# Optimization experiments

Hardware: AMD Instinct MI355X
Metric: run time of the kernel (lower is better)

Reference implementation:

```python
import jax, jax.numpy as jnp
import numpy as np

N = 50000      # nodes
E = 800000     # edges (before self loops)
NG = 512       # graphs in batch
D_IN = 128
D_H = 128
D_FC = 128
D_OUT = 2


def _gcn_conv(x, src, dst, norm, W, b, num_nodes):
    # x: [N, d_in] -> [N, d_out]; symmetric-normalized scatter-add over edges
    h = x @ W                              # [N, d_out]
    msg = h[src] * norm[:, None]           # [E+N, d_out]
    out = jax.ops.segment_sum(msg, dst, num_segments=num_nodes)
    return out + b


def setup_inputs() -> dict:
    key = jax.random.key(0)
    ks = jax.random.split(key, 12)
    x = jax.random.normal(ks[0], (N, D_IN), dtype=jnp.float32)
    edge_index = jax.random.randint(ks[1], (2, E), 0, N, dtype=jnp.int64)
    batch = jnp.sort(jax.random.randint(ks[2], (N,), 0, NG, dtype=jnp.int64))

    def glorot(k, shape):
        lim = float(np.sqrt(6.0 / (shape[0] + shape[1])))
        return jax.random.uniform(k, shape, jnp.float32, -lim, lim)

    return {
        "x": x, "edge_index": edge_index, "batch": batch,
        "W1": glorot(ks[3], (D_IN, D_H)), "b1": jnp.zeros((D_H,), jnp.float32),
        "W2": glorot(ks[4], (D_H, D_H)), "b2": jnp.zeros((D_H,), jnp.float32),
        "Wf1": glorot(ks[5], (D_H, D_FC)), "bf1": jnp.zeros((D_FC,), jnp.float32),
        "Wf2": glorot(ks[6], (D_FC, D_OUT)), "bf2": jnp.zeros((D_OUT,), jnp.float32),
    }


def reference(x, edge_index, batch, W1, b1, W2, b2, Wf1, bf1, Wf2, bf2):
    # add self loops (PyG GCNConv default)
    loops = jnp.arange(N, dtype=edge_index.dtype)
    src = jnp.concatenate([edge_index[0], loops])   # [E+N]
    dst = jnp.concatenate([edge_index[1], loops])   # [E+N]
    deg = jax.ops.segment_sum(jnp.ones_like(dst, dtype=x.dtype), dst, num_segments=N)
    dinv = jax.lax.rsqrt(deg)                       # deg >= 1 due to self loops
    norm = dinv[src] * dinv[dst]                    # [E+N]

    h = jax.nn.relu(_gcn_conv(x, src, dst, norm, W1, b1, N))
    h = jax.nn.relu(_gcn_conv(h, src, dst, norm, W2, b2, N))

    # global mean pool over graphs
    sums = jax.ops.segment_sum(h, batch, num_segments=NG)          # [NG, D_H]
    cnts = jax.ops.segment_sum(jnp.ones((N,), h.dtype), batch, num_segments=NG)
    g = sums / jnp.maximum(cnts, 1.0)[:, None]

    z = jax.nn.relu(g @ Wf1 + bf1)
    return z @ Wf2 + bf2
```

## Files before the change

### kernel.cpp

```cpp
#include <hip/hip_runtime.h>

typedef __attribute__((ext_vector_type(8))) short short8;
typedef __attribute__((ext_vector_type(4))) float f32x4;

__device__ __forceinline__ unsigned short f2b(float x) {
  unsigned u = __float_as_uint(x);
  u += 0x7FFF + ((u >> 16) & 1);
  return (unsigned short)(u >> 16);
}
__device__ __forceinline__ float b2f_lo(unsigned v) { return __uint_as_float(v << 16); }
__device__ __forceinline__ float b2f_hi(unsigned v) { return __uint_as_float(v & 0xFFFF0000u); }

#define EPB 4096
#define BKT 256
#define RPW 32

__global__ __launch_bounds__(256) void k_setup(
    const float* __restrict__ W1, unsigned short* __restrict__ Wt1,
    const float* __restrict__ W2, unsigned short* __restrict__ Wt2,
    const int* __restrict__ dst, int E, int nbuck, int* __restrict__ mat)
{
  __shared__ float tile[32][33];
  __shared__ int h[256];
  int t = threadIdx.x;
  if (blockIdx.x < 32) {
    const float* W = (blockIdx.x < 16) ? W1 : W2;
    unsigned short* Wt = (blockIdx.x < 16) ? Wt1 : Wt2;
    int bid = blockIdx.x & 15;
    int tx = t & 31, ty = t >> 5;
    int bx = bid & 3, by = bid >> 2;
    #pragma unroll
    for (int i = 0; i < 4; ++i)
      tile[ty + i * 8][tx] = W[(by * 32 + ty + i * 8) * 128 + bx * 32 + tx];
    __syncthreads();
    #pragma unroll
    for (int i = 0; i < 4; ++i)
      Wt[(bx * 32 + ty + i * 8) * 128 + by * 32 + tx] = f2b(tile[tx][ty + i * 8]);
  } else {
    int blk = blockIdx.x - 32;
    h[t] = 0;
    __syncthreads();
    int e0 = blk * EPB, e1 = min(e0 + EPB, E);
    for (int e = e0 + t; e < e1; e += 256) atomicAdd(&h[dst[e] >> 8], 1);
    __syncthreads();
    if (t < nbuck) mat[blk * nbuck + t] = h[t];
  }
}

__global__ __launch_bounds__(256) void k_excl(const int* __restrict__ mat, int neb, int nbuck,
                                              int* __restrict__ boff, int* __restrict__ cursor,
                                              int* __restrict__ rowptr, int N_) {
  __shared__ int s[256];
  int t = threadIdx.x;
  int sum = 0;
  if (t < nbuck) {
    #pragma unroll 8
    for (int r = 0; r < neb; ++r) sum += mat[r * nbuck + t];
  }
  s[t] = sum;
  __syncthreads();
  #pragma unroll
  for (int d = 1; d < 256; d <<= 1) {
    int u = (t >= d) ? s[t - d] : 0;
    __syncthreads();
    s[t] += u;
    __syncthreads();
  }
  if (t < nbuck) { boff[t] = s[t] - sum; cursor[t] = s[t] - sum; }
  if (t == 0) { boff[nbuck] = s[255]; rowptr[N_] = s[255]; }
}

__global__ __launch_bounds__(256) void k_part(const int* __restrict__ src,
                                              const int* __restrict__ dst, int E, int nbuck,
                                              const int* __restrict__ mat,
                                              int* __restrict__ cursor,
                                              unsigned* __restrict__ staged,
                                              float* __restrict__ sums,
                                              int* __restrict__ cnt, int ng) {
  __shared__ int cur[256];
  int t = threadIdx.x;
  if (t < nbuck) {
    int c = mat[blockIdx.x * nbuck + t];
    cur[t] = c ? atomicAdd(&cursor[t], c) : 0;
  }
  __syncthreads();
  int e0 = blockIdx.x * EPB, e1 = min(e0 + EPB, E);
  for (int e = e0 + t; e < e1; e += 256) {
    int d = dst[e];
    int pos = atomicAdd(&cur[d >> 8], 1);
    staged[pos] = ((unsigned)(d & 255) << 16) | (unsigned)src[e];
  }
  int tot_e = ng * 128;
  for (int i = blockIdx.x * 256 + t; i < tot_e; i += gridDim.x * 256) sums[i] = 0.f;
  for (int i = blockIdx.x * 256 + t; i < ng; i += gridDim.x * 256) cnt[i] = 0;
}

__global__ __launch_bounds__(256) void k_csr(const unsigned* __restrict__ staged,
                                             const int* __restrict__ boff, int N_,
                                             float* __restrict__ dinv, int* __restrict__ rowptr,
                                             unsigned short* __restrict__ csr16) {
  __shared__ int cnt[256];
  __shared__ int cur[256];
  int b = blockIdx.x, t = threadIdx.x;
  int lo = boff[b], hi = boff[b + 1];
  cnt[t] = 0;
  __syncthreads();
  for (int i = lo + t; i < hi; i += 256) atomicAdd(&cnt[staged[i] >> 16], 1);
  __syncthreads();
  int v = cnt[t];
  #pragma unroll
  for (int d = 1; d < 256; d <<= 1) {
    int u = (t >= d) ? cnt[t - d] : 0;
    __syncthreads();
    cnt[t] += u;
    __syncthreads();
  }
  int start = lo + cnt[t] - v;
  cur[t] = start;
  int node = (b << 8) + t;
  if (node < N_) {
    rowptr[node] = start;
    dinv[node] = rsqrtf((float)(v + 1));
  }
  __syncthreads();
  for (int i = lo + t; i < hi; i += 256) {
    unsigned e = staged[i];
    int pos = atomicAdd(&cur[e >> 16], 1);
    csr16[pos] = (unsigned short)(e & 0xFFFFu);
  }
}

template<int A_F32>
__global__ __launch_bounds__(256) void k_mfma_gemm(
    const void* __restrict__ Ap, const unsigned short* __restrict__ Wt,
    const float* __restrict__ dinv, unsigned short* __restrict__ Out, int M)
{
  int wv = threadIdx.x >> 6, lane = threadIdx.x & 63;
  int kb = (lane >> 4) * 8;
  short8 bf[8][4];
  const unsigned short* Bc = Wt + (size_t)(lane & 15) * 128 + kb;
  #pragma unroll
  for (int ct = 0; ct < 8; ++ct)
    #pragma unroll
    for (int ks = 0; ks < 4; ++ks)
      bf[ct][ks] = *(const short8*)(Bc + ct * 16 * 128 + ks * 32);

  int r0 = (blockIdx.x * 4 + wv) * 32;
  #pragma unroll
  for (int rt = 0; rt < 2; ++rt) {
    int rbase = r0 + rt * 16;
    if (rbase >= M) return;
    int arow = rbase + (lane & 15);
    short8 a[4];
    if (A_F32) {
      const float* Ar = (const float*)Ap + (size_t)arow * 128 + kb;
      #pragma unroll
      for (int ks = 0; ks < 4; ++ks) {
        float4 u = *(const float4*)(Ar + ks * 32);
        float4 v = *(const float4*)(Ar + ks * 32 + 4);
        short8 tt;
        tt[0] = (short)f2b(u.x); tt[1] = (short)f2b(u.y);
        tt[2] = (short)f2b(u.z); tt[3] = (short)f2b(u.w);
        tt[4] = (short)f2b(v.x); tt[5] = (short)f2b(v.y);
        tt[6] = (short)f2b(v.z); tt[7] = (short)f2b(v.w);
        a[ks] = tt;
      }
    } else {
      const unsigned short* Ar = (const unsigned short*)Ap + (size_t)arow * 128 + kb;
      #pragma unroll
      for (int ks = 0; ks < 4; ++ks)
        a[ks] = *(const short8*)(Ar + ks * 32);
    }
    f32x4 acc[8];
    #pragma unroll
    for (int i = 0; i < 8; ++i) acc[i] = (f32x4){0.f, 0.f, 0.f, 0.f};
    #pragma unroll
    for (int ct = 0; ct < 8; ++ct)
      #pragma unroll
      for (int ks = 0; ks < 4; ++ks)
        acc[ct] = __builtin_amdgcn_mfma_f32_16x16x32_bf16(a[ks], bf[ct][ks], acc[ct], 0, 0, 0);
    int orow = rbase + (lane >> 4) * 4;
    int ocol = lane & 15;
    float s0 = dinv[orow], s1 = dinv[orow + 1], s2 = dinv[orow + 2], s3 = dinv[orow + 3];
    #pragma unroll
    for (int ct = 0; ct < 8; ++ct) {
      unsigned short* o = Out + (size_t)orow * 128 + ct * 16 + ocol;
      o[0]   = f2b(acc[ct][0] * s0);
      o[128] = f2b(acc[ct][1] * s1);
      o[256] = f2b(acc[ct][2] * s2);
      o[384] = f2b(acc[ct][3] * s3);
    }
  }
}

__global__ __launch_bounds__(256) void k_gather_post(
    const unsigned short* __restrict__ csr16, const int* __restrict__ rowptr,
    const unsigned short* __restrict__ P, const float* __restrict__ dinv,
    const float* __restrict__ bias, unsigned short* __restrict__ R, int n)
{
  int node = blockIdx.x * 8 + (threadIdx.x >> 5);
  if (node >= n) return;
  int lane = threadIdx.x & 31;
  int lo = rowptr[node], hi = rowptr[node + 1];
  float a0 = 0.f, a1 = 0.f, a2 = 0.f, a3 = 0.f;
  int e = lo;
  for (; e + 8 <= hi; e += 8) {
    int s0 = csr16[e],     s1 = csr16[e + 1], s2 = csr16[e + 2], s3 = csr16[e + 3];
    int s4 = csr16[e + 4], s5 = csr16[e + 5], s6 = csr16[e + 6], s7 = csr16[e + 7];
    uint2 v0 = ((const uint2*)(P + (size_t)s0 * 128))[lane];
    uint2 v1 = ((const uint2*)(P + (size_t)s1 * 128))[lane];
    uint2 v2 = ((const uint2*)(P + (size_t)s2 * 128))[lane];
    uint2 v3 = ((const uint2*)(P + (size_t)s3 * 128))[lane];
    uint2 v4 = ((const uint2*)(P + (size_t)s4 * 128))[lane];
    uint2 v5 = ((const uint2*)(P + (size_t)s5 * 128))[lane];
    uint2 v6 = ((const uint2*)(P + (size_t)s6 * 128))[lane];
    uint2 v7 = ((const uint2*)(P + (size_t)s7 * 128))[lane];
    a0 += b2f_lo(v0.x) + b2f_lo(v1.x) + b2f_lo(v2.x) + b2f_lo(v3.x)
        + b2f_lo(v4.x) + b2f_lo(v5.x) + b2f_lo(v6.x) + b2f_lo(v7.x);
    a1 += b2f_hi(v0.x) + b2f_hi(v1.x) + b2f_hi(v2.x) + b2f_hi(v3.x)
        + b2f_hi(v4.x) + b2f_hi(v5.x) + b2f_hi(v6.x) + b2f_hi(v7.x);
    a2 += b2f_lo(v0.y) + b2f_lo(v1.y) + b2f_lo(v2.y) + b2f_lo(v3.y)
        + b2f_lo(v4.y) + b2f_lo(v5.y) + b2f_lo(v6.y) + b2f_lo(v7.y);
    a3 += b2f_hi(v0.y) + b2f_hi(v1.y) + b2f_hi(v2.y) + b2f_hi(v3.y)
        + b2f_hi(v4.y) + b2f_hi(v5.y) + b2f_hi(v6.y) + b2f_hi(v7.y);
  }
  for (; e + 4 <= hi; e += 4) {
    int s0 = csr16[e], s1 = csr16[e + 1], s2 = csr16[e + 2], s3 = csr16[e + 3];
    uint2 v0 = ((const uint2*)(P + (size_t)s0 * 128))[lane];
    uint2 v1 = ((const uint2*)(P + (size_t)s1 * 128))[lane];
    uint2 v2 = ((const uint2*)(P + (size_t)s2 * 128))[lane];
    uint2 v3 = ((const uint2*)(P + (size_t)s3 * 128))[lane];
    a0 += b2f_lo(v0.x) + b2f_lo(v1.x) + b2f_lo(v2.x) + b2f_lo(v3.x);
    a1 += b2f_hi(v0.x) + b2f_hi(v1.x) + b2f_hi(v2.x) + b2f_hi(v3.x);
    a2 += b2f_lo(v0.y) + b2f_lo(v1.y) + b2f_lo(v2.y) + b2f_lo(v3.y);
    a3 += b2f_hi(v0.y) + b2f_hi(v1.y) + b2f_hi(v2.y) + b2f_hi(v3.y);
  }
  for (; e < hi; ++e) {
    int s = csr16[e];
    uint2 v = ((const uint2*)(P + (size_t)s * 128))[lane];
    a0 += b2f_lo(v.x); a1 += b2f_hi(v.x);
    a2 += b2f_lo(v.y); a3 += b2f_hi(v.y);
  }
  float dv = dinv[node];
  uint2 hv = ((const uint2*)(P + (size_t)node * 128))[lane];
  float4 bb = ((const float4*)bias)[lane];
  float r0 = fmaxf(dv * (a0 + b2f_lo(hv.x)) + bb.x, 0.f);
  float r1 = fmaxf(dv * (a1 + b2f_hi(hv.x)) + bb.y, 0.f);
  float r2 = fmaxf(dv * (a2 + b2f_lo(hv.y)) + bb.z, 0.f);
  float r3 = fmaxf(dv * (a3 + b2f_hi(hv.y)) + bb.w, 0.f);
  uint2 pack;
  pack.x = (unsigned)f2b(r0) | ((unsigned)f2b(r1) << 16);
  pack.y = (unsigned)f2b(r2) | ((unsigned)f2b(r3) << 16);
  ((uint2*)(R + (size_t)node * 128))[lane] = pack;
}

__global__ __launch_bounds__(256) void k_pool_sum(
    const unsigned short* __restrict__ h2, const int* __restrict__ batch, int n,
    float* __restrict__ sums, int* __restrict__ cnt)
{
  int wid = blockIdx.x * 4 + (threadIdx.x >> 6);
  int lane = threadIdx.x & 63;
  int r0 = wid * RPW;
  if (r0 >= n) return;
  int r1 = min(r0 + RPW, n);
  const unsigned* H = (const unsigned*)h2;
  int gcur = batch[r0];
  float ax = 0.f, ay = 0.f;
  int run = 0;
  for (int r = r0; r < r1; ++r) {
    int g = batch[r];
    if (g != gcur) {
      atomicAdd(&sums[(size_t)gcur * 128 + 2 * lane], ax);
      atomicAdd(&sums[(size_t)gcur * 128 + 2 * lane + 1], ay);
      if (lane == 0) atomicAdd(&cnt[gcur], run);
      ax = ay = 0.f; run = 0; gcur = g;
    }
    unsigned v = H[(size_t)r * 64 + lane];
    ax += b2f_lo(v); ay += b2f_hi(v); ++run;
  }
  atomicAdd(&sums[(size_t)gcur * 128 + 2 * lane], ax);
  atomicAdd(&sums[(size_t)gcur * 128 + 2 * lane + 1], ay);
  if (lane == 0) atomicAdd(&cnt[gcur], run);
}

__global__ __launch_bounds__(128) void k_fc(
    const float* __restrict__ sums, const int* __restrict__ cnt,
    const float* __restrict__ Wf1, const float* __restrict__ bf1,
    const float* __restrict__ Wf2, const float* __restrict__ bf2,
    float* __restrict__ out)
{
  __shared__ float gl[128];
  __shared__ float red0[128];
  __shared__ float red1[128];
  int g = blockIdx.x, t = threadIdx.x;
  float c = (float)cnt[g];
  gl[t] = sums[(size_t)g * 128 + t] / fmaxf(c, 1.f);
  __syncthreads();
  float z0 = 0.f, z1 = 0.f, z2 = 0.f, z3 = 0.f;
  #pragma unroll
  for (int k = 0; k < 32; ++k) {
    z0 += gl[k]      * Wf1[k * 128 + t];
    z1 += gl[k + 32] * Wf1[(k + 32) * 128 + t];
    z2 += gl[k + 64] * Wf1[(k + 64) * 128 + t];
    z3 += gl[k + 96] * Wf1[(k + 96) * 128 + t];
  }
  float z = fmaxf((z0 + z1) + (z2 + z3) + bf1[t], 0.f);
  red0[t] = z * Wf2[2 * t];
  red1[t] = z * Wf2[2 * t + 1];
  __syncthreads();
  #pragma unroll
  for (int d = 64; d > 0; d >>= 1) {
    if (t < d) { red0[t] += red0[t + d]; red1[t] += red1[t + d]; }
    __syncthreads();
  }
  if (t == 0) {
    out[g * 2]     = red0[0] + bf2[0];
    out[g * 2 + 1] = red1[0] + bf2[1];
  }
}

extern "C" void kernel_launch(void* const* d_in, const int* in_sizes, int n_in,
                              void* d_out, int out_size, void* d_ws, size_t ws_size,
                              hipStream_t stream) {
  const float* x    = (const float*)d_in[0];
  const int*   ei   = (const int*)d_in[1];
  const int*   batch= (const int*)d_in[2];
  const float* W1   = (const float*)d_in[3];
  const float* b1   = (const float*)d_in[4];
  const float* W2   = (const float*)d_in[5];
  const float* b2   = (const float*)d_in[6];
  const float* Wf1  = (const float*)d_in[7];
  const float* bf1  = (const float*)d_in[8];
  const float* Wf2  = (const float*)d_in[9];
  const float* bf2  = (const float*)d_in[10];
  float* out = (float*)d_out;

  const int N  = in_sizes[0] / 128;
  const int E  = in_sizes[1] / 2;
  const int NG = out_size / 2;
  const int* srcp = ei;
  const int* dstp = ei + E;

  const int nbuck = (N + BKT - 1) / BKT;
  const int neb   = (E + EPB - 1) / EPB;

  char* ws = (char*)d_ws;
  size_t off = 0;
  auto carve = [&](size_t bytes) { void* p = ws + off; off += (bytes + 255) & ~(size_t)255; return p; };
  float* dinv   = (float*)carve((size_t)N * 4);
  int*   rowptr = (int*)  carve((size_t)(N + 1) * 4);
  int*   boff   = (int*)  carve((size_t)(nbuck + 1) * 4);
  int*   cursor = (int*)  carve((size_t)256 * 4);
  int*   mat    = (int*)  carve((size_t)neb * nbuck * 4);
  unsigned*       staged = (unsigned*)      carve((size_t)E * 4);
  unsigned short* csr16  = (unsigned short*)carve((size_t)E * 2);
  unsigned short* Wt1 = (unsigned short*)carve(128 * 128 * 2);
  unsigned short* Wt2 = (unsigned short*)carve(128 * 128 * 2);
  float* sums   = (float*)carve((size_t)NG * 128 * 4);
  int*   cntg   = (int*)  carve((size_t)NG * 4);
  const size_t nb_row = (size_t)N * 128 * 2;
  unsigned short* U0 = (unsigned short*)carve(nb_row);
  unsigned short* U1 = (unsigned short*)carve(nb_row);

  k_setup<<<32 + neb, 256, 0, stream>>>(W1, Wt1, W2, Wt2, dstp, E, nbuck, mat);
  k_excl<<<1, 256, 0, stream>>>(mat, neb, nbuck, boff, cursor, rowptr, N);
  k_part<<<neb, 256, 0, stream>>>(srcp, dstp, E, nbuck, mat, cursor, staged, sums, cntg, NG);
  k_csr <<<nbuck, 256, 0, stream>>>(staged, boff, N, dinv, rowptr, csr16);

  const int gblocks = (N + 127) / 128;
  k_mfma_gemm<1><<<gblocks, 256, 0, stream>>>(x, Wt1, dinv, U0, N);
  k_gather_post<<<(N + 7) / 8, 256, 0, stream>>>(csr16, rowptr, U0, dinv, b1, U1, N);
  k_mfma_gemm<0><<<gblocks, 256, 0, stream>>>(U1, Wt2, dinv, U0, N);
  k_gather_post<<<(N + 7) / 8, 256, 0, stream>>>(csr16, rowptr, U0, dinv, b2, U1, N);

  const int pblocks = (N + RPW * 4 - 1) / (RPW * 4);
  k_pool_sum<<<pblocks, 256, 0, stream>>>(U1, batch, N, sums, cntg);
  k_fc<<<NG, 128, 0, stream>>>(sums, cntg, Wf1, bf1, Wf2, bf2, out);
}
```

Baseline: 160.9 us.

## Fuse CSR build stages into one cooperative kernel with grid syncs

Replaces the four graph-preprocessing launches (bucket histogram/weight transpose, scan, partition, per-bucket CSR) with a single cooperative kernel of 256 blocks that loops over the former block indices and separates stages with grid.sync(). The goal is to remove three kernel launch gaps and their inter-kernel drain. In exchange, each stage now runs on a fixed 256-block grid, so the stages that had more blocks get less parallelism, and the scan stage runs on one block while the rest wait at a grid barrier.

After: 256.9 us. +59.7%, slower.

```diff
diff --git a/kernel.cpp b/kernel.cpp
--- a/kernel.cpp
+++ b/kernel.cpp
@@ -1,4 +1,7 @@
 #include <hip/hip_runtime.h>
+#include <hip/hip_cooperative_groups.h>
+
+namespace cg = cooperative_groups;
 
 typedef __attribute__((ext_vector_type(8))) short short8;
 typedef __attribute__((ext_vector_type(4))) float f32x4;
@@ -15,118 +18,119 @@
 #define BKT 256
 #define RPW 32
 
-__global__ __launch_bounds__(256) void k_setup(
+__global__ __launch_bounds__(256) void k_build(
     const float* __restrict__ W1, unsigned short* __restrict__ Wt1,
     const float* __restrict__ W2, unsigned short* __restrict__ Wt2,
-    const int* __restrict__ dst, int E, int nbuck, int* __restrict__ mat)
-{
+    const int* __restrict__ src, const int* __restrict__ dst,
+    int E, int N_, int nbuck, int neb,
+    int* __restrict__ mat, int* __restrict__ boff, int* __restrict__ cursor,
+    int* __restrict__ rowptr, unsigned* __restrict__ staged,
+    unsigned short* __restrict__ csr16, float* __restrict__ dinv,
+    float* __restrict__ sums, int* __restrict__ cntg, int ng)
+{
+  cg::grid_group grid = cg::this_grid();
   __shared__ float tile[32][33];
-  __shared__ int h[256];
-  int t = threadIdx.x;
-  if (blockIdx.x < 32) {
-    const float* W = (blockIdx.x < 16) ? W1 : W2;
-    unsigned short* Wt = (blockIdx.x < 16) ? Wt1 : Wt2;
-    int bid = blockIdx.x & 15;
-    int tx = t & 31, ty = t >> 5;
-    int bx = bid & 3, by = bid >> 2;
-    #pragma unroll
-    for (int i = 0; i < 4; ++i)
-      tile[ty + i * 8][tx] = W[(by * 32 + ty + i * 8) * 128 + bx * 32 + tx];
-    __syncthreads();
-    #pragma unroll
-    for (int i = 0; i < 4; ++i)
-      Wt[(bx * 32 + ty + i * 8) * 128 + by * 32 + tx] = f2b(tile[tx][ty + i * 8]);
-  } else {
-    int blk = blockIdx.x - 32;
-    h[t] = 0;
-    __syncthreads();
-    int e0 = blk * EPB, e1 = min(e0 + EPB, E);
-    for (int e = e0 + t; e < e1; e += 256) atomicAdd(&h[dst[e] >> 8], 1);
-    __syncthreads();
-    if (t < nbuck) mat[blk * nbuck + t] = h[t];
-  }
-}
-
-__global__ __launch_bounds__(256) void k_excl(const int* __restrict__ mat, int neb, int nbuck,
-                                              int* __restrict__ boff, int* __restrict__ cursor,
-                                              int* __restrict__ rowptr, int N_) {
-  __shared__ int s[256];
-  int t = threadIdx.x;
-  int sum = 0;
-  if (t < nbuck) {
-    #pragma unroll 8
-    for (int r = 0; r < neb; ++r) sum += mat[r * nbuck + t];
-  }
-  s[t] = sum;
-  __syncthreads();
-  #pragma unroll
-  for (int d = 1; d < 256; d <<= 1) {
-    int u = (t >= d) ? s[t - d] : 0;
-    __syncthreads();
-    s[t] += u;
-    __syncthreads();
-  }
-  if (t < nbuck) { boff[t] = s[t] - sum; cursor[t] = s[t] - sum; }
-  if (t == 0) { boff[nbuck] = s[255]; rowptr[N_] = s[255]; }
-}
-
-__global__ __launch_bounds__(256) void k_part(const int* __restrict__ src,
-                                              const int* __restrict__ dst, int E, int nbuck,
-                                              const int* __restrict__ mat,
-                                              int* __restrict__ cursor,
-                                              unsigned* __restrict__ staged,
-                                              float* __restrict__ sums,
-                                              int* __restrict__ cnt, int ng) {
-  __shared__ int cur[256];
-  int t = threadIdx.x;
-  if (t < nbuck) {
-    int c = mat[blockIdx.x * nbuck + t];
-    cur[t] = c ? atomicAdd(&cursor[t], c) : 0;
-  }
-  __syncthreads();
-  int e0 = blockIdx.x * EPB, e1 = min(e0 + EPB, E);
-  for (int e = e0 + t; e < e1; e += 256) {
-    int d = dst[e];
-    int pos = atomicAdd(&cur[d >> 8], 1);
-    staged[pos] = ((unsigned)(d & 255) << 16) | (unsigned)src[e];
-  }
-  int tot_e = ng * 128;
-  for (int i = blockIdx.x * 256 + t; i < tot_e; i += gridDim.x * 256) sums[i] = 0.f;
-  for (int i = blockIdx.x * 256 + t; i < ng; i += gridDim.x * 256) cnt[i] = 0;
-}
-
-__global__ __launch_bounds__(256) void k_csr(const unsigned* __restrict__ staged,
-                                             const int* __restrict__ boff, int N_,
-                                             float* __restrict__ dinv, int* __restrict__ rowptr,
-                                             unsigned short* __restrict__ csr16) {
-  __shared__ int cnt[256];
-  __shared__ int cur[256];
-  int b = blockIdx.x, t = threadIdx.x;
-  int lo = boff[b], hi = boff[b + 1];
-  cnt[t] = 0;
-  __syncthreads();
-  for (int i = lo + t; i < hi; i += 256) atomicAdd(&cnt[staged[i] >> 16], 1);
-  __syncthreads();
-  int v = cnt[t];
-  #pragma unroll
-  for (int d = 1; d < 256; d <<= 1) {
-    int u = (t >= d) ? cnt[t - d] : 0;
-    __syncthreads();
-    cnt[t] += u;
-    __syncthreads();
-  }
-  int start = lo + cnt[t] - v;
-  cur[t] = start;
-  int node = (b << 8) + t;
-  if (node < N_) {
-    rowptr[node] = start;
-    dinv[node] = rsqrtf((float)(v + 1));
-  }
-  __syncthreads();
-  for (int i = lo + t; i < hi; i += 256) {
-    unsigned e = staged[i];
-    int pos = atomicAdd(&cur[e >> 16], 1);
-    csr16[pos] = (unsigned short)(e & 0xFFFFu);
+  __shared__ int ibuf[256];
+  __shared__ int ibuf2[256];
+  const int t = threadIdx.x;
+
+  for (int b = blockIdx.x; b < 32 + neb; b += gridDim.x) {
+    if (b < 32) {
+      const float* W = (b < 16) ? W1 : W2;
+      unsigned short* Wt = (b < 16) ? Wt1 : Wt2;
+      int bid = b & 15;
+      int tx = t & 31, ty = t >> 5;
+      int bx = bid & 3, by = bid >> 2;
+      #pragma unroll
+      for (int i = 0; i < 4; ++i)
+        tile[ty + i * 8][tx] = W[(by * 32 + ty + i * 8) * 128 + bx * 32 + tx];
+      __syncthreads();
+      #pragma unroll
+      for (int i = 0; i < 4; ++i)
+        Wt[(bx * 32 + ty + i * 8) * 128 + by * 32 + tx] = f2b(tile[tx][ty + i * 8]);
+      __syncthreads();
+    } else {
+      int blk = b - 32;
+      ibuf[t] = 0;
+      __syncthreads();
+      int e0 = blk * EPB, e1 = min(e0 + EPB, E);
+      for (int e = e0 + t; e < e1; e += 256) atomicAdd(&ibuf[dst[e] >> 8], 1);
+      __syncthreads();
+      if (t < nbuck) mat[blk * nbuck + t] = ibuf[t];
+      __syncthreads();
+    }
+  }
+  grid.sync();
+
+  if (blockIdx.x == 0) {
+    int sum = 0;
+    if (t < nbuck) {
+      #pragma unroll 8
+      for (int r = 0; r < neb; ++r) sum += mat[r * nbuck + t];
+    }
+    ibuf[t] = sum;
+    __syncthreads();
+    #pragma unroll
+    for (int d = 1; d < 256; d <<= 1) {
+      int u = (t >= d) ? ibuf[t - d] : 0;
+      __syncthreads();
+      ibuf[t] += u;
+      __syncthreads();
+    }
+    if (t < nbuck) { boff[t] = ibuf[t] - sum; cursor[t] = ibuf[t] - sum; }
+    if (t == 0) { boff[nbuck] = ibuf[255]; rowptr[N_] = ibuf[255]; }
+  }
+  grid.sync();
+
+  for (int b = blockIdx.x; b < neb; b += gridDim.x) {
+    __syncthreads();
+    if (t < nbuck) {
+      int c = mat[b * nbuck + t];
+      ibuf2[t] = c ? atomicAdd(&cursor[t], c) : 0;
+    }
+    __syncthreads();
+    int e0 = b * EPB, e1 = min(e0 + EPB, E);
+    for (int e = e0 + t; e < e1; e += 256) {
+      int d = dst[e];
+      int pos = atomicAdd(&ibuf2[d >> 8], 1);
+      staged[pos] = ((unsigned)(d & 255) << 16) | (unsigned)src[e];
+    }
+  }
+  {
+    int tot_e = ng * 128;
+    for (int i = blockIdx.x * 256 + t; i < tot_e; i += gridDim.x * 256) sums[i] = 0.f;
+    for (int i = blockIdx.x * 256 + t; i < ng; i += gridDim.x * 256) cntg[i] = 0;
+  }
+  grid.sync();
+
+  for (int b = blockIdx.x; b < nbuck; b += gridDim.x) {
+    __syncthreads();
+    int lo = boff[b], hi = boff[b + 1];
+    ibuf[t] = 0;
+    __syncthreads();
+    for (int i = lo + t; i < hi; i += 256) atomicAdd(&ibuf[staged[i] >> 16], 1);
+    __syncthreads();
+    int v = ibuf[t];
+    #pragma unroll
+    for (int d = 1; d < 256; d <<= 1) {
+      int u = (t >= d) ? ibuf[t - d] : 0;
+      __syncthreads();
+      ibuf[t] += u;
+      __syncthreads();
+    }
+    int start = lo + ibuf[t] - v;
+    ibuf2[t] = start;
+    int node = (b << 8) + t;
+    if (node < N_) {
+      rowptr[node] = start;
+      dinv[node] = rsqrtf((float)(v + 1));
+    }
+    __syncthreads();
+    for (int i = lo + t; i < hi; i += 256) {
+      unsigned e = staged[i];
+      int pos = atomicAdd(&ibuf2[e >> 16], 1);
+      csr16[pos] = (unsigned short)(e & 0xFFFFu);
+    }
   }
 }
 
@@ -362,10 +366,16 @@
   unsigned short* U0 = (unsigned short*)carve(nb_row);
   unsigned short* U1 = (unsigned short*)carve(nb_row);
 
-  k_setup<<<32 + neb, 256, 0, stream>>>(W1, Wt1, W2, Wt2, dstp, E, nbuck, mat);
-  k_excl<<<1, 256, 0, stream>>>(mat, neb, nbuck, boff, cursor, rowptr, N);
-  k_part<<<neb, 256, 0, stream>>>(srcp, dstp, E, nbuck, mat, cursor, staged, sums, cntg, NG);
-  k_csr <<<nbuck, 256, 0, stream>>>(staged, boff, N, dinv, rowptr, csr16);
+  {
+    int E_ = E, N_ = N, nbuck_ = nbuck, neb_ = neb, ng_ = NG;
+    void* args[] = {
+      (void*)&W1, (void*)&Wt1, (void*)&W2, (void*)&Wt2,
+      (void*)&srcp, (void*)&dstp, (void*)&E_, (void*)&N_, (void*)&nbuck_, (void*)&neb_,
+      (void*)&mat, (void*)&boff, (void*)&cursor, (void*)&rowptr,
+      (void*)&staged, (void*)&csr16, (void*)&dinv, (void*)&sums, (void*)&cntg, (void*)&ng_
+    };
+    hipLaunchCooperativeKernel((void*)k_build, dim3(256), dim3(256), args, 0, stream);
+  }
 
   const int gblocks = (N + 127) / 128;
   k_mfma_gemm<1><<<gblocks, 256, 0, stream>>>(x, Wt1, dinv, U0, N);
```

## Fuse second gather layer with global mean pooling via shared-memory accumulation

Applied to the files above, without the earlier changes.

The second GCN aggregation is merged with the graph mean-pool. Each node's ReLU output is accumulated into a per-block shared-memory partial sum for the block's first graph, and into global sums through atomics otherwise. This drops the bf16 write and re-read of the second hidden layer and one kernel launch. In exchange it adds shared atomics, global atomics at graph boundaries, and a change in summation order that affects float results.

After: 172.1 us. 6.9% more time.

```diff
diff --git a/kernel.cpp b/kernel.cpp
--- a/kernel.cpp
+++ b/kernel.cpp
@@ -13,7 +13,6 @@
 
 #define EPB 4096
 #define BKT 256
-#define RPW 32
 
 __global__ __launch_bounds__(256) void k_setup(
     const float* __restrict__ W1, unsigned short* __restrict__ Wt1,
@@ -193,16 +192,10 @@
   }
 }
 
-__global__ __launch_bounds__(256) void k_gather_post(
-    const unsigned short* __restrict__ csr16, const int* __restrict__ rowptr,
-    const unsigned short* __restrict__ P, const float* __restrict__ dinv,
-    const float* __restrict__ bias, unsigned short* __restrict__ R, int n)
-{
-  int node = blockIdx.x * 8 + (threadIdx.x >> 5);
-  if (node >= n) return;
-  int lane = threadIdx.x & 31;
-  int lo = rowptr[node], hi = rowptr[node + 1];
-  float a0 = 0.f, a1 = 0.f, a2 = 0.f, a3 = 0.f;
+__device__ __forceinline__ void gather_row(
+    const unsigned short* __restrict__ csr16, const unsigned short* __restrict__ P,
+    int lo, int hi, int lane, float& a0, float& a1, float& a2, float& a3)
+{
   int e = lo;
   for (; e + 8 <= hi; e += 8) {
     int s0 = csr16[e],     s1 = csr16[e + 1], s2 = csr16[e + 2], s3 = csr16[e + 3];
@@ -241,6 +234,19 @@
     a0 += b2f_lo(v.x); a1 += b2f_hi(v.x);
     a2 += b2f_lo(v.y); a3 += b2f_hi(v.y);
   }
+}
+
+__global__ __launch_bounds__(256) void k_gather_post(
+    const unsigned short* __restrict__ csr16, const int* __restrict__ rowptr,
+    const unsigned short* __restrict__ P, const float* __restrict__ dinv,
+    const float* __restrict__ bias, unsigned short* __restrict__ R, int n)
+{
+  int node = blockIdx.x * 8 + (threadIdx.x >> 5);
+  if (node >= n) return;
+  int lane = threadIdx.x & 31;
+  int lo = rowptr[node], hi = rowptr[node + 1];
+  float a0 = 0.f, a1 = 0.f, a2 = 0.f, a3 = 0.f;
+  gather_row(csr16, P, lo, hi, lane, a0, a1, a2, a3);
   float dv = dinv[node];
   uint2 hv = ((const uint2*)(P + (size_t)node * 128))[lane];
   float4 bb = ((const float4*)bias)[lane];
@@ -254,33 +260,56 @@
   ((uint2*)(R + (size_t)node * 128))[lane] = pack;
 }
 
-__global__ __launch_bounds__(256) void k_pool_sum(
-    const unsigned short* __restrict__ h2, const int* __restrict__ batch, int n,
-    float* __restrict__ sums, int* __restrict__ cnt)
-{
-  int wid = blockIdx.x * 4 + (threadIdx.x >> 6);
-  int lane = threadIdx.x & 63;
-  int r0 = wid * RPW;
-  if (r0 >= n) return;
-  int r1 = min(r0 + RPW, n);
-  const unsigned* H = (const unsigned*)h2;
-  int gcur = batch[r0];
-  float ax = 0.f, ay = 0.f;
-  int run = 0;
-  for (int r = r0; r < r1; ++r) {
-    int g = batch[r];
-    if (g != gcur) {
-      atomicAdd(&sums[(size_t)gcur * 128 + 2 * lane], ax);
-      atomicAdd(&sums[(size_t)gcur * 128 + 2 * lane + 1], ay);
-      if (lane == 0) atomicAdd(&cnt[gcur], run);
-      ax = ay = 0.f; run = 0; gcur = g;
+__global__ __launch_bounds__(256) void k_gather_pool(
+    const unsigned short* __restrict__ csr16, const int* __restrict__ rowptr,
+    const unsigned short* __restrict__ P, const float* __restrict__ dinv,
+    const float* __restrict__ bias, const int* __restrict__ batch,
+    float* __restrict__ sums, int* __restrict__ cnt, int n)
+{
+  __shared__ float bsum[128];
+  __shared__ int bcnt;
+  int hw = threadIdx.x >> 5;
+  int node = (int)blockIdx.x * 8 + hw;
+  int lane = threadIdx.x & 31;
+  if (threadIdx.x < 128) bsum[threadIdx.x] = 0.f;
+  if (threadIdx.x == 0) bcnt = 0;
+  __syncthreads();
+  int gidx = (int)blockIdx.x * 8;
+  if (gidx > n - 1) gidx = n - 1;
+  int g_first = batch[gidx];
+  if (node < n) {
+    int lo = rowptr[node], hi = rowptr[node + 1];
+    float a0 = 0.f, a1 = 0.f, a2 = 0.f, a3 = 0.f;
+    gather_row(csr16, P, lo, hi, lane, a0, a1, a2, a3);
+    float dv = dinv[node];
+    uint2 hv = ((const uint2*)(P + (size_t)node * 128))[lane];
+    float4 bb = ((const float4*)bias)[lane];
+    float r0 = fmaxf(dv * (a0 + b2f_lo(hv.x)) + bb.x, 0.f);
+    float r1 = fmaxf(dv * (a1 + b2f_hi(hv.x)) + bb.y, 0.f);
+    float r2 = fmaxf(dv * (a2 + b2f_lo(hv.y)) + bb.z, 0.f);
+    float r3 = fmaxf(dv * (a3 + b2f_hi(hv.y)) + bb.w, 0.f);
+    int g = batch[node];
+    if (g == g_first) {
+      atomicAdd(&bsum[lane * 4 + 0], r0);
+      atomicAdd(&bsum[lane * 4 + 1], r1);
+      atomicAdd(&bsum[lane * 4 + 2], r2);
+      atomicAdd(&bsum[lane * 4 + 3], r3);
+      if (lane == 0) atomicAdd(&bcnt, 1);
+    } else {
+      float* sg = sums + (size_t)g * 128 + lane * 4;
+      atomicAdd(sg + 0, r0);
+      atomicAdd(sg + 1, r1);
+      atomicAdd(sg + 2, r2);
+      atomicAdd(sg + 3, r3);
+      if (lane == 0) atomicAdd(&cnt[g], 1);
     }
-    unsigned v = H[(size_t)r * 64 + lane];
-    ax += b2f_lo(v); ay += b2f_hi(v); ++run;
-  }
-  atomicAdd(&sums[(size_t)gcur * 128 + 2 * lane], ax);
-  atomicAdd(&sums[(size_t)gcur * 128 + 2 * lane + 1], ay);
-  if (lane == 0) atomicAdd(&cnt[gcur], run);
+  }
+  __syncthreads();
+  if (threadIdx.x < 128) {
+    float v = bsum[threadIdx.x];
+    if (v != 0.f) atomicAdd(&sums[(size_t)g_first * 128 + threadIdx.x], v);
+  }
+  if (threadIdx.x == 0 && bcnt) atomicAdd(&cnt[g_first], bcnt);
 }
 
 __global__ __launch_bounds__(128) void k_fc(
@@ -371,9 +400,7 @@
   k_mfma_gemm<1><<<gblocks, 256, 0, stream>>>(x, Wt1, dinv, U0, N);
   k_gather_post<<<(N + 7) / 8, 256, 0, stream>>>(csr16, rowptr, U0, dinv, b1, U1, N);
   k_mfma_gemm<0><<<gblocks, 256, 0, stream>>>(U1, Wt2, dinv, U0, N);
-  k_gather_post<<<(N + 7) / 8, 256, 0, stream>>>(csr16, rowptr, U0, dinv, b2, U1, N);
-
-  const int pblocks = (N + RPW * 4 - 1) / (RPW * 4);
-  k_pool_sum<<<pblocks, 256, 0, stream>>>(U1, batch, N, sums, cntg);
+  k_gather_pool<<<(N + 7) / 8, 256, 0, stream>>>(csr16, rowptr, U0, dinv, b2, batch,
+                                                 sums, cntg, N);
   k_fc<<<NG, 128, 0, stream>>>(sums, cntg, Wf1, bf1, Wf2, bf2, out);
 }
```

## Split gather aggregation into four feature slices across adjacent blocks

Applied to the files above, without the earlier changes.

The neighbor-gather kernel now splits each node's 128 features into four 32-feature slices. Adjacent blocks (blockIdx & 3) each handle one slice for the same 16 nodes, with 16 lanes per node each loading 4 bytes. The aim is to shrink the working set per block and raise parallelism, so that concurrently running blocks touching the same source rows may share cache lines. The cost is four times more index reads and rowptr lookups, plus narrower 4-byte loads per lane.

Result: slower. 187.0 us (+16.2%).

```diff
diff --git a/kernel.cpp b/kernel.cpp
--- a/kernel.cpp
+++ b/kernel.cpp
@@ -193,65 +193,55 @@
   }
 }
 
-__global__ __launch_bounds__(256) void k_gather_post(
+__global__ __launch_bounds__(256) void k_gather_slice(
     const unsigned short* __restrict__ csr16, const int* __restrict__ rowptr,
     const unsigned short* __restrict__ P, const float* __restrict__ dinv,
     const float* __restrict__ bias, unsigned short* __restrict__ R, int n)
 {
-  int node = blockIdx.x * 8 + (threadIdx.x >> 5);
+  int s = blockIdx.x & 3;
+  int node = (blockIdx.x >> 2) * 16 + (threadIdx.x >> 4);
   if (node >= n) return;
-  int lane = threadIdx.x & 31;
+  int l = threadIdx.x & 15;
+  const unsigned* Ps = (const unsigned*)P + s * 16;
   int lo = rowptr[node], hi = rowptr[node + 1];
-  float a0 = 0.f, a1 = 0.f, a2 = 0.f, a3 = 0.f;
+  float a0 = 0.f, a1 = 0.f;
   int e = lo;
   for (; e + 8 <= hi; e += 8) {
     int s0 = csr16[e],     s1 = csr16[e + 1], s2 = csr16[e + 2], s3 = csr16[e + 3];
     int s4 = csr16[e + 4], s5 = csr16[e + 5], s6 = csr16[e + 6], s7 = csr16[e + 7];
-    uint2 v0 = ((const uint2*)(P + (size_t)s0 * 128))[lane];
-    uint2 v1 = ((const uint2*)(P + (size_t)s1 * 128))[lane];
-    uint2 v2 = ((const uint2*)(P + (size_t)s2 * 128))[lane];
-    uint2 v3 = ((const uint2*)(P + (size_t)s3 * 128))[lane];
-    uint2 v4 = ((const uint2*)(P + (size_t)s4 * 128))[lane];
-    uint2 v5 = ((const uint2*)(P + (size_t)s5 * 128))[lane];
-    uint2 v6 = ((const uint2*)(P + (size_t)s6 * 128))[lane];
-    uint2 v7 = ((const uint2*)(P + (size_t)s7 * 128))[lane];
-    a0 += b2f_lo(v0.x) + b2f_lo(v1.x) + b2f_lo(v2.x) + b2f_lo(v3.x)
-        + b2f_lo(v4.x) + b2f_lo(v5.x) + b2f_lo(v6.x) + b2f_lo(v7.x);
-    a1 += b2f_hi(v0.x) + b2f_hi(v1.x) + b2f_hi(v2.x) + b2f_hi(v3.x)
-        + b2f_hi(v4.x) + b2f_hi(v5.x) + b2f_hi(v6.x) + b2f_hi(v7.x);
-    a2 += b2f_lo(v0.y) + b2f_lo(v1.y) + b2f_lo(v2.y) + b2f_lo(v3.y)
-        + b2f_lo(v4.y) + b2f_lo(v5.y) + b2f_lo(v6.y) + b2f_lo(v7.y);
-    a3 += b2f_hi(v0.y) + b2f_hi(v1.y) + b2f_hi(v2.y) + b2f_hi(v3.y)
-        + b2f_hi(v4.y) + b2f_hi(v5.y) + b2f_hi(v6.y) + b2f_hi(v7.y);
+    unsigned v0 = Ps[(size_t)s0 * 64 + l];
+    unsigned v1 = Ps[(size_t)s1 * 64 + l];
+    unsigned v2 = Ps[(size_t)s2 * 64 + l];
+    unsigned v3 = Ps[(size_t)s3 * 64 + l];
+    unsigned v4 = Ps[(size_t)s4 * 64 + l];
+    unsigned v5 = Ps[(size_t)s5 * 64 + l];
+    unsigned v6 = Ps[(size_t)s6 * 64 + l];
+    unsigned v7 = Ps[(size_t)s7 * 64 + l];
+    a0 += b2f_lo(v0) + b2f_lo(v1) + b2f_lo(v2) + b2f_lo(v3)
+        + b2f_lo(v4) + b2f_lo(v5) + b2f_lo(v6) + b2f_lo(v7);
+    a1 += b2f_hi(v0) + b2f_hi(v1) + b2f_hi(v2) + b2f_hi(v3)
+        + b2f_hi(v4) + b2f_hi(v5) + b2f_hi(v6) + b2f_hi(v7);
   }
   for (; e + 4 <= hi; e += 4) {
     int s0 = csr16[e], s1 = csr16[e + 1], s2 = csr16[e + 2], s3 = csr16[e + 3];
-    uint2 v0 = ((const uint2*)(P + (size_t)s0 * 128))[lane];
-    uint2 v1 = ((const uint2*)(P + (size_t)s1 * 128))[lane];
-    uint2 v2 = ((const uint2*)(P + (size_t)s2 * 128))[lane];
-    uint2 v3 = ((const uint2*)(P + (size_t)s3 * 128))[lane];
-    a0 += b2f_lo(v0.x) + b2f_lo(v1.x) + b2f_lo(v2.x) + b2f_lo(v3.x);
-    a1 += b2f_hi(v0.x) + b2f_hi(v1.x) + b2f_hi(v2.x) + b2f_hi(v3.x);
-    a2 += b2f_lo(v0.y) + b2f_lo(v1.y) + b2f_lo(v2.y) + b2f_lo(v3.y);
-    a3 += b2f_hi(v0.y) + b2f_hi(v1.y) + b2f_hi(v2.y) + b2f_hi(v3.y);
+    unsigned v0 = Ps[(size_t)s0 * 64 + l];
+    unsigned v1 = Ps[(size_t)s1 * 64 + l];
+    unsigned v2 = Ps[(size_t)s2 * 64 + l];
+    unsigned v3 = Ps[(size_t)s3 * 64 + l];
+    a0 += b2f_lo(v0) + b2f_lo(v1) + b2f_lo(v2) + b2f_lo(v3);
+    a1 += b2f_hi(v0) + b2f_hi(v1) + b2f_hi(v2) + b2f_hi(v3);
   }
   for (; e < hi; ++e) {
-    int s = csr16[e];
-    uint2 v = ((const uint2*)(P + (size_t)s * 128))[lane];
-    a0 += b2f_lo(v.x); a1 += b2f_hi(v.x);
-    a2 += b2f_lo(v.y); a3 += b2f_hi(v.y);
+    unsigned v = Ps[(size_t)csr16[e] * 64 + l];
+    a0 += b2f_lo(v); a1 += b2f_hi(v);
   }
   float dv = dinv[node];
-  uint2 hv = ((const uint2*)(P + (size_t)node * 128))[lane];
-  float4 bb = ((const float4*)bias)[lane];
-  float r0 = fmaxf(dv * (a0 + b2f_lo(hv.x)) + bb.x, 0.f);
-  float r1 = fmaxf(dv * (a1 + b2f_hi(hv.x)) + bb.y, 0.f);
-  float r2 = fmaxf(dv * (a2 + b2f_lo(hv.y)) + bb.z, 0.f);
-  float r3 = fmaxf(dv * (a3 + b2f_hi(hv.y)) + bb.w, 0.f);
-  uint2 pack;
-  pack.x = (unsigned)f2b(r0) | ((unsigned)f2b(r1) << 16);
-  pack.y = (unsigned)f2b(r2) | ((unsigned)f2b(r3) << 16);
-  ((uint2*)(R + (size_t)node * 128))[lane] = pack;
+  unsigned hv = Ps[(size_t)node * 64 + l];
+  float2 bb = ((const float2*)bias)[s * 16 + l];
+  float r0 = fmaxf(dv * (a0 + b2f_lo(hv)) + bb.x, 0.f);
+  float r1 = fmaxf(dv * (a1 + b2f_hi(hv)) + bb.y, 0.f);
+  unsigned pack = (unsigned)f2b(r0) | ((unsigned)f2b(r1) << 16);
+  ((unsigned*)R)[(size_t)node * 64 + s * 16 + l] = pack;
 }
 
 __global__ __launch_bounds__(256) void k_pool_sum(
@@ -368,10 +358,11 @@
   k_csr <<<nbuck, 256, 0, stream>>>(staged, boff, N, dinv, rowptr, csr16);
 
   const int gblocks = (N + 127) / 128;
+  const int sblocks = 4 * ((N + 15) / 16);
   k_mfma_gemm<1><<<gblocks, 256, 0, stream>>>(x, Wt1, dinv, U0, N);
-  k_gather_post<<<(N + 7) / 8, 256, 0, stream>>>(csr16, rowptr, U0, dinv, b1, U1, N);
+  k_gather_slice<<<sblocks, 256, 0, stream>>>(csr16, rowptr, U0, dinv, b1, U1, N);
   k_mfma_gemm<0><<<gblocks, 256, 0, stream>>>(U1, Wt2, dinv, U0, N);
-  k_gather_post<<<(N + 7) / 8, 256, 0, stream>>>(csr16, rowptr, U0, dinv, b2, U1, N);
+  k_gather_slice<<<sblocks, 256, 0, stream>>>(csr16, rowptr, U0, dinv, b2, U1, N);
 
   const int pblocks = (N + RPW * 4 - 1) / (RPW * 4);
   k_pool_sum<<<pblocks, 256, 0, stream>>>(U1, batch, N, sums, cntg);
```
